# Optimization experiments

Hardware: AMD Instinct MI355X
Metric: run time of the kernel (lower is better)

Reference implementation:

```python
import jax, jax.numpy as jnp
import numpy as np
from jax import lax

K_NEIGHBORS = 10  # topk k=10 in pool_lig
BN_EPS = 1e-5


def setup_inputs() -> dict:
    key = jax.random.key(0)
    ks = jax.random.split(key, 8)
    B, N, L, D, OUT = 32, 32768, 64, 128, 7
    return {
        "pos": jax.random.normal(ks[0], (B, N, 3), jnp.float32) * 10.0,
        "x": jax.random.normal(ks[1], (B, N, D), jnp.float32),
        "lig_coords": jax.random.normal(ks[2], (B, L, 3), jnp.float32) * 10.0,
        "W1": jax.random.normal(ks[3], (D, D), jnp.float32) / np.sqrt(D),
        "b1": jnp.zeros((D,), jnp.float32),
        "gamma": jnp.ones((D,), jnp.float32),
        "beta": jnp.zeros((D,), jnp.float32),
        "run_mean": jnp.zeros((D,), jnp.float32),
        "run_var": jnp.ones((D,), jnp.float32),
        "W2": jax.random.normal(ks[4], (D, OUT), jnp.float32) / np.sqrt(D),
        "b2": jnp.zeros((OUT,), jnp.float32),
    }


def _pool_lig(p, feats, lig):
    # p: [N,3], feats: [N,D], lig: [L,3]
    # squared cdist via GEMM expansion (monotone in true distance, so topk indices match)
    d2 = (p * p).sum(-1)[:, None] + (lig * lig).sum(-1)[None, :] - 2.0 * p @ lig.T  # [N,L]
    d2 = lax.stop_gradient(d2)  # torch.no_grad() in pool_lig
    _, idx = lax.top_k(-d2.T, K_NEIGHBORS)  # [L,K] nearest-vertex indices per ligand atom
    # unique(): collapse duplicates via a membership mask over vertices
    mask = jnp.zeros((p.shape[0],), feats.dtype).at[idx.reshape(-1)].set(1.0)  # [N]
    # mean over the unique selected vertices
    return (feats * mask[:, None]).sum(0) / mask.sum()  # [D]


def reference(pos, x, lig_coords, W1, b1, gamma, beta, run_mean, run_var, W2, b2):
    emb = jax.vmap(_pool_lig)(pos, x, lig_coords)  # [B,D] pocket embeddings
    # top_net: Linear -> Dropout(eval=id) -> BatchNorm1d(eval) -> SiLU -> Linear
    h = emb @ W1 + b1
    h = (h - run_mean) / jnp.sqrt(run_var + BN_EPS) * gamma + beta
    h = jax.nn.silu(h)
    return h @ W2 + b2
```

## Files before the change

kernel.cpp:

```cpp
#include <hip/hip_runtime.h>
#include <math.h>

#define B_    32
#define NV    32768
#define LA    64
#define DIM   128
#define OUTD  7
#define TOPK  10
#define CHUNK 1024
#define NCH   (NV / CHUNK)
#define NMW   (NV / 32)
#define MAXU  (LA * TOPK)
#define NSEG  16
#define LCAP  24

typedef unsigned long long u64;

__global__ void k1_threshold(const float* __restrict__ pos,
                             const float* __restrict__ lig,
                             float* __restrict__ T, unsigned int* __restrict__ cnt,
                             unsigned int* __restrict__ maskG) {
  const int l = blockIdx.x, b = blockIdx.y;
  const int lane = threadIdx.x;
  const int bl = b * LA + l;
  if (lane == 0) cnt[bl] = 0u;
  if (lane >= 32 && lane < 48) maskG[b * NMW + l * 16 + (lane - 32)] = 0u;
  const float lx = lig[bl * 3 + 0];
  const float ly = lig[bl * 3 + 1];
  const float lz = lig[bl * 3 + 2];
  const float* pb = pos + (size_t)b * NV * 3;
  float d2a[16];
#pragma unroll
  for (int k = 0; k < 16; ++k) {
    int v = lane + 64 * k;
    float dx = pb[v * 3 + 0] - lx;
    float dy = pb[v * 3 + 1] - ly;
    float dz = pb[v * 3 + 2] - lz;
    d2a[k] = fmaf(dx, dx, fmaf(dy, dy, dz * dz));
  }
  float s[TOPK];
#pragma unroll
  for (int i = 0; i < TOPK; ++i) s[i] = INFINITY;
#pragma unroll
  for (int k = 0; k < 16; ++k) {
    float d2 = d2a[k];
    if (d2 < s[TOPK - 1]) {
      s[TOPK - 1] = d2;
#pragma unroll
      for (int i = TOPK - 1; i >= 1; --i)
        if (s[i] < s[i - 1]) { float t = s[i]; s[i] = s[i - 1]; s[i - 1] = t; }
    }
  }
  float T10 = 0.f;
  for (int r = 0; r < TOPK; ++r) {
    float v = s[0];
#pragma unroll
    for (int o = 1; o < 64; o <<= 1) v = fminf(v, __shfl_xor(v, o, 64));
    T10 = v;
    if (s[0] == v) {
#pragma unroll
      for (int i = 0; i < TOPK - 1; ++i) s[i] = s[i + 1];
      s[TOPK - 1] = INFINITY;
    }
  }
  if (lane == 0) T[bl] = T10;
}

__global__ void k2_filter(const float* __restrict__ pos,
                          const float* __restrict__ lig,
                          const float* __restrict__ T,
                          unsigned int* __restrict__ cnt,
                          u64* __restrict__ cand, int cap) {
  __shared__ float4 vp[CHUNK];
  __shared__ u64 lcand[LA][LCAP];
  __shared__ unsigned lcnt[LA];
  __shared__ unsigned gbaseS[LA];
  const int c = blockIdx.x, b = blockIdx.y;
  const int tid = threadIdx.x;
  const int base = c * CHUNK;
  const float* pb = pos + ((size_t)b * NV + base) * 3;
  for (int j = tid; j < CHUNK * 3; j += 1024) {
    int v = j / 3, comp = j - 3 * v;
    float val = pb[j];
    if (comp == 0) vp[v].x = val;
    else if (comp == 1) vp[v].y = val;
    else vp[v].z = val;
  }
  if (tid < LA) lcnt[tid] = 0u;
  __syncthreads();
  for (int v = tid; v < CHUNK; v += 1024) {
    float px = vp[v].x, py = vp[v].y, pz = vp[v].z;
    vp[v].w = fmaf(px, px, fmaf(py, py, pz * pz));
  }
  __syncthreads();
  const int lg = tid >> 4, vl = tid & 15;
  const int l = lg;
  float lx = lig[(b * LA + l) * 3 + 0];
  float ly = lig[(b * LA + l) * 3 + 1];
  float lz = lig[(b * LA + l) * 3 + 2];
  const float Ax = -2.f * lx, Ay = -2.f * ly, Az = -2.f * lz;
  const float Cl = lx * lx + ly * ly + lz * lz;
  const float TH = T[b * LA + l] + 0.01f - Cl;
  for (int k = 0; k < CHUNK / 16; ++k) {
    int v = vl + 16 * k;
    float4 p = vp[v];
    float t = fmaf(p.x, Ax, fmaf(p.y, Ay, fmaf(p.z, Az, p.w)));
    if (t <= TH) {
      float d2 = fmaxf(t + Cl, 0.f);
      u64 key = ((u64)__float_as_uint(d2) << 32) | (unsigned)(base + v);
      unsigned p2 = atomicAdd(&lcnt[l], 1u);
      if (p2 < (unsigned)LCAP) lcand[l][p2] = key;
      else {
        unsigned pidx = atomicAdd(&cnt[b * LA + l], 1u);
        if (pidx < (unsigned)cap) cand[(size_t)(b * LA + l) * cap + pidx] = key;
      }
    }
  }
  __syncthreads();
  if (tid < LA) {
    int mcount = (int)min(lcnt[tid], (unsigned)LCAP);
    gbaseS[tid] = (mcount > 0) ? atomicAdd(&cnt[b * LA + tid], (unsigned)mcount) : 0u;
  }
  __syncthreads();
  for (int idx = tid; idx < LA * LCAP; idx += 1024) {
    const int ll = idx / LCAP, i = idx - ll * LCAP;
    if (i < (int)min(lcnt[ll], (unsigned)LCAP)) {
      unsigned g = gbaseS[ll] + (unsigned)i;
      if (g < (unsigned)cap) cand[(size_t)(b * LA + ll) * cap + g] = lcand[ll][i];
    }
  }
}

__global__ void k3_select(const unsigned int* __restrict__ cnt,
                          const u64* __restrict__ cand, int cap,
                          unsigned int* __restrict__ maskG) {
  const int bl = blockIdx.x;
  const int b = bl / LA;
  const int lane = threadIdx.x;
  int n = (int)min(cnt[bl], (unsigned)cap);
  u64 s[TOPK];
#pragma unroll
  for (int i = 0; i < TOPK; ++i) s[i] = 0xFFFFFFFFFFFFFFFFull;
  for (int i = lane; i < n; i += 64) {
    u64 key = cand[(size_t)bl * cap + i];
    if (key < s[TOPK - 1]) {
      s[TOPK - 1] = key;
#pragma unroll
      for (int i2 = TOPK - 1; i2 >= 1; --i2)
        if (s[i2] < s[i2 - 1]) { u64 t = s[i2]; s[i2] = s[i2 - 1]; s[i2 - 1] = t; }
    }
  }
  int prev = 0, myidx = 0;
  for (int r = 0; r < TOPK; ++r) {
    u64 v = s[0];
#pragma unroll
    for (int o = 1; o < 64; o <<= 1) {
      u64 other = __shfl_xor(v, o, 64);
      v = (other < v) ? other : v;
    }
    if (s[0] == v) {
#pragma unroll
      for (int i = 0; i < TOPK - 1; ++i) s[i] = s[i + 1];
      s[TOPK - 1] = 0xFFFFFFFFFFFFFFFFull;
    }
    int idx = (int)(unsigned)(v & 0xFFFFFFFFu);
    if ((v >> 32) == 0xFFFFFFFFull) idx = prev;
    prev = idx;
    if (lane == r) myidx = idx;
  }
  if (lane < TOPK)
    atomicOr(&maskG[b * NMW + (myidx >> 5)], 1u << (myidx & 31));
}

__global__ void k4a_gather(const float* __restrict__ x,
                           const unsigned int* __restrict__ maskG,
                           int* __restrict__ cntU,
                           double* __restrict__ partial) {
  __shared__ int list[MAXU];
  __shared__ int wtot[8], wbase[8];
  __shared__ int cntS;
  __shared__ double red[4][DIM];
  const int seg = blockIdx.x, b = blockIdx.y, tid = threadIdx.x;
  const int w = tid >> 6, lane = tid & 63;
  unsigned wd[2];
  int c = 0;
#pragma unroll
  for (int k = 0; k < 2; ++k) {
    wd[k] = maskG[b * NMW + tid * 2 + k];
    c += __popc(wd[k]);
  }
  int incl = c;
#pragma unroll
  for (int o = 1; o < 64; o <<= 1) {
    int up = __shfl_up(incl, o, 64);
    if (lane >= o) incl += up;
  }
  if (lane == 63) wtot[w] = incl;
  __syncthreads();
  if (tid == 0) {
    int s = 0;
#pragma unroll
    for (int i = 0; i < 8; ++i) { wbase[i] = s; s += wtot[i]; }
    cntS = s;
  }
  __syncthreads();
  int p = wbase[w] + incl - c;
#pragma unroll
  for (int k = 0; k < 2; ++k) {
    unsigned bits = wd[k];
    while (bits) {
      int bit = __ffs(bits) - 1;
      list[p++] = (tid * 2 + k) * 32 + bit;
      bits &= bits - 1;
    }
  }
  __syncthreads();
  const int n = cntS;
  if (seg == 0 && tid == 0) cntU[b] = n;
  const int r0 = (seg * n) / NSEG, r1 = ((seg + 1) * n) / NSEG;
  const int slot = tid >> 7, col = tid & 127;
  const float* xb = x + (size_t)b * NV * DIM;
  double a0 = 0, a1 = 0, a2 = 0, a3 = 0, a4 = 0, a5 = 0, a6 = 0, a7 = 0;
  int i = r0 + slot;
  for (; i + 28 < r1; i += 32) {
    float v0 = xb[(size_t)list[i +  0] * DIM + col];
    float v1 = xb[(size_t)list[i +  4] * DIM + col];
    float v2 = xb[(size_t)list[i +  8] * DIM + col];
    float v3 = xb[(size_t)list[i + 12] * DIM + col];
    float v4 = xb[(size_t)list[i + 16] * DIM + col];
    float v5 = xb[(size_t)list[i + 20] * DIM + col];
    float v6 = xb[(size_t)list[i + 24] * DIM + col];
    float v7 = xb[(size_t)list[i + 28] * DIM + col];
    a0 += (double)v0; a1 += (double)v1; a2 += (double)v2; a3 += (double)v3;
    a4 += (double)v4; a5 += (double)v5; a6 += (double)v6; a7 += (double)v7;
  }
  for (; i < r1; i += 4) a0 += (double)xb[(size_t)list[i] * DIM + col];
  red[slot][col] = (((a0 + a1) + (a2 + a3)) + ((a4 + a5) + (a6 + a7)));
  __syncthreads();
  if (tid < DIM)
    partial[((size_t)b * NSEG + seg) * DIM + tid] =
        (red[0][tid] + red[1][tid]) + (red[2][tid] + red[3][tid]);
}

__global__ void k4b_mlp(const double* __restrict__ partial,
                        const int* __restrict__ cntU,
                        const float* __restrict__ W1, const float* __restrict__ b1,
                        const float* __restrict__ gamma, const float* __restrict__ beta,
                        const float* __restrict__ rm, const float* __restrict__ rv,
                        const float* __restrict__ W2, const float* __restrict__ b2,
                        float* __restrict__ out) {
  __shared__ float embS[DIM];
  __shared__ float hpart[4][DIM];
  __shared__ float hS[DIM];
  const int b = blockIdx.x, t = threadIdx.x;
  if (t < DIM) {
    double s = 0;
#pragma unroll
    for (int seg = 0; seg < NSEG; ++seg)
      s += partial[((size_t)b * NSEG + seg) * DIM + t];
    embS[t] = (float)(s / (double)cntU[b]);
  }
  __syncthreads();
  {
    const int d = t & 127, q = t >> 7;
    float hp = 0.f;
    const int dd0 = q * 32;
#pragma unroll 8
    for (int dd = dd0; dd < dd0 + 32; ++dd) hp = fmaf(embS[dd], W1[dd * DIM + d], hp);
    hpart[q][d] = hp;
  }
  __syncthreads();
  if (t < DIM) {
    float h = ((hpart[0][t] + hpart[1][t]) + (hpart[2][t] + hpart[3][t])) + b1[t];
    h = (h - rm[t]) / sqrtf(rv[t] + 1e-5f) * gamma[t] + beta[t];
    h = h / (1.f + expf(-h));
    hS[t] = h;
  }
  __syncthreads();
  if (t < OUTD * 16) {
    const int o = t >> 4, g = t & 15;
    float p = 0.f;
#pragma unroll
    for (int dd = g * 8; dd < g * 8 + 8; ++dd) p = fmaf(hS[dd], W2[dd * OUTD + o], p);
#pragma unroll
    for (int off = 8; off >= 1; off >>= 1) p += __shfl_down(p, off, 16);
    if (g == 0) out[b * OUTD + o] = p + b2[o];
  }
}

extern "C" void kernel_launch(void* const* d_in, const int* in_sizes, int n_in,
                              void* d_out, int out_size, void* d_ws, size_t ws_size,
                              hipStream_t stream) {
  const float* pos  = (const float*)d_in[0];
  const float* x    = (const float*)d_in[1];
  const float* lig  = (const float*)d_in[2];
  const float* W1   = (const float*)d_in[3];
  const float* b1   = (const float*)d_in[4];
  const float* gam  = (const float*)d_in[5];
  const float* bet  = (const float*)d_in[6];
  const float* rm   = (const float*)d_in[7];
  const float* rv   = (const float*)d_in[8];
  const float* W2   = (const float*)d_in[9];
  const float* b2   = (const float*)d_in[10];
  float* out = (float*)d_out;

  char* ws = (char*)d_ws;
  const int NBL = B_ * LA;
  float* T            = (float*)(ws);
  unsigned int* cnt   = (unsigned int*)(ws + 8192);
  unsigned int* maskG = (unsigned int*)(ws + 16384);
  int* cntU           = (int*)(ws + 147456);
  double* partial     = (double*)(ws + 147584);
  u64* cand           = (u64*)(ws + 671872);
  size_t fixed = 671872;
  size_t avail = ws_size > fixed ? ws_size - fixed : 0;
  int cap = (int)(avail / ((size_t)NBL * 8));
  if (cap > 1024) cap = 1024;
  if (cap < 16) cap = 16;

  k1_threshold<<<dim3(LA, B_), 64, 0, stream>>>(pos, lig, T, cnt, maskG);
  k2_filter<<<dim3(NCH, B_), 1024, 0, stream>>>(pos, lig, T, cnt, cand, cap);
  k3_select<<<NBL, 64, 0, stream>>>(cnt, cand, cap, maskG);
  k4a_gather<<<dim3(NSEG, B_), 512, 0, stream>>>(x, maskG, cntU, partial);
  k4b_mlp<<<B_, 512, 0, stream>>>(partial, cntU, W1, b1, gam, bet, rm, rv, W2, b2, out);
}
```

Before: 62.75 us.

## Restructure filter kernel: 256 threads, vertices in registers, loop over ligand atoms

The filter kernel drops from 1024 to 256 threads per block. Each thread keeps 4 vertices (with precomputed squared norms) in registers and loops over all 64 ligand atoms, whose coefficients and thresholds are staged once in shared memory. This removes the separate norm pass and one barrier, and cuts repeated shared-memory vertex reads. The cost is a longer serial loop per thread and fewer waves to hide latency.

```diff
diff --git a/kernel.cpp b/kernel.cpp
--- a/kernel.cpp
+++ b/kernel.cpp
@@ -72,6 +72,8 @@
                           unsigned int* __restrict__ cnt,
                           u64* __restrict__ cand, int cap) {
   __shared__ float4 vp[CHUNK];
+  __shared__ float4 ligA[LA];
+  __shared__ float  ligTH[LA];
   __shared__ u64 lcand[LA][LCAP];
   __shared__ unsigned lcnt[LA];
   __shared__ unsigned gbaseS[LA];
@@ -79,40 +81,47 @@
   const int tid = threadIdx.x;
   const int base = c * CHUNK;
   const float* pb = pos + ((size_t)b * NV + base) * 3;
-  for (int j = tid; j < CHUNK * 3; j += 1024) {
+  for (int j = tid; j < CHUNK * 3; j += 256) {
     int v = j / 3, comp = j - 3 * v;
     float val = pb[j];
     if (comp == 0) vp[v].x = val;
     else if (comp == 1) vp[v].y = val;
     else vp[v].z = val;
   }
-  if (tid < LA) lcnt[tid] = 0u;
-  __syncthreads();
-  for (int v = tid; v < CHUNK; v += 1024) {
-    float px = vp[v].x, py = vp[v].y, pz = vp[v].z;
-    vp[v].w = fmaf(px, px, fmaf(py, py, pz * pz));
-  }
-  __syncthreads();
-  const int lg = tid >> 4, vl = tid & 15;
-  const int l = lg;
-  float lx = lig[(b * LA + l) * 3 + 0];
-  float ly = lig[(b * LA + l) * 3 + 1];
-  float lz = lig[(b * LA + l) * 3 + 2];
-  const float Ax = -2.f * lx, Ay = -2.f * ly, Az = -2.f * lz;
-  const float Cl = lx * lx + ly * ly + lz * lz;
-  const float TH = T[b * LA + l] + 0.01f - Cl;
-  for (int k = 0; k < CHUNK / 16; ++k) {
-    int v = vl + 16 * k;
-    float4 p = vp[v];
-    float t = fmaf(p.x, Ax, fmaf(p.y, Ay, fmaf(p.z, Az, p.w)));
-    if (t <= TH) {
-      float d2 = fmaxf(t + Cl, 0.f);
-      u64 key = ((u64)__float_as_uint(d2) << 32) | (unsigned)(base + v);
-      unsigned p2 = atomicAdd(&lcnt[l], 1u);
-      if (p2 < (unsigned)LCAP) lcand[l][p2] = key;
-      else {
-        unsigned pidx = atomicAdd(&cnt[b * LA + l], 1u);
-        if (pidx < (unsigned)cap) cand[(size_t)(b * LA + l) * cap + pidx] = key;
+  if (tid < LA) {
+    const int l = tid;
+    float lx = lig[(b * LA + l) * 3 + 0];
+    float ly = lig[(b * LA + l) * 3 + 1];
+    float lz = lig[(b * LA + l) * 3 + 2];
+    float Cl = lx * lx + ly * ly + lz * lz;
+    ligA[l] = make_float4(-2.f * lx, -2.f * ly, -2.f * lz, Cl);
+    ligTH[l] = T[b * LA + l] + 0.01f - Cl;
+    lcnt[l] = 0u;
+  }
+  __syncthreads();
+  float4 P[4];
+#pragma unroll
+  for (int k = 0; k < 4; ++k) {
+    float4 p = vp[tid + 256 * k];
+    p.w = fmaf(p.x, p.x, fmaf(p.y, p.y, p.z * p.z));
+    P[k] = p;
+  }
+  for (int l = 0; l < LA; ++l) {
+    float4 A = ligA[l];
+    float th = ligTH[l];
+#pragma unroll
+    for (int k = 0; k < 4; ++k) {
+      float t = fmaf(P[k].x, A.x, fmaf(P[k].y, A.y, fmaf(P[k].z, A.z, P[k].w)));
+      if (t <= th) {
+        float d2 = fmaxf(t + A.w, 0.f);
+        int v = base + tid + 256 * k;
+        u64 key = ((u64)__float_as_uint(d2) << 32) | (unsigned)v;
+        unsigned p2 = atomicAdd(&lcnt[l], 1u);
+        if (p2 < (unsigned)LCAP) lcand[l][p2] = key;
+        else {
+          unsigned pidx = atomicAdd(&cnt[b * LA + l], 1u);
+          if (pidx < (unsigned)cap) cand[(size_t)(b * LA + l) * cap + pidx] = key;
+        }
       }
     }
   }
@@ -122,7 +131,7 @@
     gbaseS[tid] = (mcount > 0) ? atomicAdd(&cnt[b * LA + tid], (unsigned)mcount) : 0u;
   }
   __syncthreads();
-  for (int idx = tid; idx < LA * LCAP; idx += 1024) {
+  for (int idx = tid; idx < LA * LCAP; idx += 256) {
     const int ll = idx / LCAP, i = idx - ll * LCAP;
     if (i < (int)min(lcnt[ll], (unsigned)LCAP)) {
       unsigned g = gbaseS[ll] + (unsigned)i;
@@ -319,7 +328,7 @@
   if (cap < 16) cap = 16;
 
   k1_threshold<<<dim3(LA, B_), 64, 0, stream>>>(pos, lig, T, cnt, maskG);
-  k2_filter<<<dim3(NCH, B_), 1024, 0, stream>>>(pos, lig, T, cnt, cand, cap);
+  k2_filter<<<dim3(NCH, B_), 256, 0, stream>>>(pos, lig, T, cnt, cand, cap);
   k3_select<<<NBL, 64, 0, stream>>>(cnt, cand, cap, maskG);
   k4a_gather<<<dim3(NSEG, B_), 512, 0, stream>>>(x, maskG, cntU, partial);
   k4b_mlp<<<B_, 512, 0, stream>>>(partial, cntU, W1, b1, gam, bet, rm, rv, W2, b2, out);
```

New measurement: 71.18 us. 13.4% more time.
